# Performance work log

Measured on AMD Instinct MI355X. Metric: run time of the kernel, lower is better.

## Reference

```python
import jax, jax.numpy as jnp
import numpy as np

NUM_HEADS = 16
PROJECT_DIM = 1024
HEAD_DIM = PROJECT_DIM // NUM_HEADS  # 64; used only for the softmax scale


def setup_inputs() -> dict:
    key = jax.random.key(0)
    k1, k2, k3 = jax.random.split(key, 3)
    B, N, D = 8, 3072, PROJECT_DIM
    inputs = jax.random.normal(k1, (B, N, D), dtype=jnp.float32)
    wqkv = jax.random.normal(k2, (D, 3 * D), dtype=jnp.float32) * (1.0 / np.sqrt(D))
    dense_w = jax.random.normal(k3, (3 * D, D), dtype=jnp.float32) * (1.0 / np.sqrt(3 * D))
    dense_b = jnp.zeros((D,), dtype=jnp.float32)
    return {"inputs": inputs, "wqkv": wqkv, "dense_w": dense_w, "dense_b": dense_b}


def reference(inputs, wqkv, dense_w, dense_b):
    B, N, D = inputs.shape
    H = NUM_HEADS
    # fused QKV projection: [B, N, 3D]
    qkv = jnp.einsum('bnd,de->bne', inputs, wqkv)
    # separate heads: [B, H, N, 3*head_dim]
    qkv = qkv.reshape(B, N, H, (3 * D) // H).transpose(0, 2, 1, 3)
    # NOTE: faithful to source — split along TOKEN axis (axis=2) into 3 chunks
    q, k, v = jnp.split(qkv, 3, axis=2)  # each [B, H, N//3, 3*head_dim]
    scale = 1.0 / jnp.sqrt(jnp.float32(HEAD_DIM))
    logits = jnp.einsum('bhqc,bhkc->bhqk', q, k) * scale  # [B, H, N//3, N//3]
    attn = jax.nn.softmax(logits, axis=-1)
    out = jnp.einsum('bhqk,bhkc->bhqc', attn, v)  # [B, H, N//3, 3*head_dim]
    # recombine heads -> [B, N//3, 3D]
    out = out.transpose(0, 2, 1, 3).reshape(B, N // 3, 3 * D)
    # output projection -> [B, N//3, D]
    return jnp.einsum('bnc,cd->bnd', out, dense_w) + dense_b
```

## Files before the change

kernel.cpp:

```cpp
#include <hip/hip_runtime.h>
#include <hip/hip_bf16.h>

typedef unsigned short u16;
using f32x4  = __attribute__((ext_vector_type(4))) float;
using bf16x8 = __attribute__((ext_vector_type(8))) short;

typedef __attribute__((address_space(1))) const void global_cvoid;
typedef __attribute__((address_space(3))) void lds_void;

__device__ __forceinline__ void async16(const u16* g, u16* l) {
    __builtin_amdgcn_global_load_lds((global_cvoid*)g, (lds_void*)l, 16, 0, 0);
}

__device__ __forceinline__ u16 f2bf(float f) {
    union { float f; unsigned u; } cv; cv.f = f;
    unsigned r = cv.u + 0x7fff + ((cv.u >> 16) & 1);
    return (u16)(r >> 16);
}

__device__ __forceinline__ u16 f2bf_rz(float f) {
    union { float f; unsigned u; } cv; cv.f = f;
    return (u16)(cv.u >> 16);
}

__device__ __forceinline__ float dppmax16(float x) {
    union { float f; int i; } c, o;
    c.f = x;
    o.i = __builtin_amdgcn_update_dpp(0, c.i, 0xB1,  0xF, 0xF, true); c.f = fmaxf(c.f, o.f);
    o.i = __builtin_amdgcn_update_dpp(0, c.i, 0x4E,  0xF, 0xF, true); c.f = fmaxf(c.f, o.f);
    o.i = __builtin_amdgcn_update_dpp(0, c.i, 0x141, 0xF, 0xF, true); c.f = fmaxf(c.f, o.f);
    o.i = __builtin_amdgcn_update_dpp(0, c.i, 0x140, 0xF, 0xF, true); c.f = fmaxf(c.f, o.f);
    return c.f;
}
__device__ __forceinline__ float dppsum16(float x) {
    union { float f; int i; } c, o;
    c.f = x;
    o.i = __builtin_amdgcn_update_dpp(0, c.i, 0xB1,  0xF, 0xF, true); c.f += o.f;
    o.i = __builtin_amdgcn_update_dpp(0, c.i, 0x4E,  0xF, 0xF, true); c.f += o.f;
    o.i = __builtin_amdgcn_update_dpp(0, c.i, 0x141, 0xF, 0xF, true); c.f += o.f;
    o.i = __builtin_amdgcn_update_dpp(0, c.i, 0x140, 0xF, 0xF, true); c.f += o.f;
    return c.f;
}

__global__ __launch_bounds__(256) void cast_kernel(const float* __restrict__ src,
                                                   u16* __restrict__ dst, int n4) {
    int i = blockIdx.x * blockDim.x + threadIdx.x;
    int st = gridDim.x * blockDim.x;
    for (; i < n4; i += st) {
        float4 v = ((const float4*)src)[i];
        ushort4 o;
        o.x = f2bf(v.x); o.y = f2bf(v.y); o.z = f2bf(v.z); o.w = f2bf(v.w);
        ((ushort4*)dst)[i] = o;
    }
}

__global__ __launch_bounds__(256) void wtrans_kernel(const float* __restrict__ src,
                                                     u16* __restrict__ dst, int R, int C) {
    __shared__ float tile[64][68];
    int ct = blockIdx.x, rt = blockIdx.y;
    int t = threadIdx.x;
    int r = t >> 2;
    const float* s = src + (size_t)(rt * 64 + r) * C + ct * 64;
#pragma unroll
    for (int jj = 0; jj < 4; ++jj) {
        int c4 = (t & 3) + jj * 4;
        float4 v = *(const float4*)(s + c4 * 4);
        *(float4*)&tile[r][c4 * 4] = v;
    }
    __syncthreads();
    int od = t >> 2;
    u16* d = dst + (size_t)(ct * 64 + od) * R + rt * 64;
#pragma unroll
    for (int jj = 0; jj < 4; ++jj) {
        int c4 = (t & 3) + jj * 4;
        ushort4 v;
        v.x = f2bf(tile[c4 * 4 + 0][od]);
        v.y = f2bf(tile[c4 * 4 + 1][od]);
        v.z = f2bf(tile[c4 * 4 + 2][od]);
        v.w = f2bf(tile[c4 * 4 + 3][od]);
        *(ushort4*)(d + c4 * 4) = v;
    }
}

template<bool OUT_F32>
__global__ __launch_bounds__(256, 2)
void gemm_bt_kernel(const u16* __restrict__ A, const u16* __restrict__ BT,
                    void* __restrict__ Cout, const float* __restrict__ bias,
                    u16* __restrict__ VTout,
                    int M, int N, int K) {
    __shared__ u16 lA[128 * 64];
    __shared__ u16 lB[128 * 64];
    const int t = threadIdx.x;
    const int w = t >> 6, lane = t & 63;
    const int nbx = N >> 7;
    const int nwg = gridDim.x;
    int bid = blockIdx.x;
    int cpx = nwg >> 3;
    int swz = (bid & 7) * cpx + (bid >> 3);
    const int bx = swz % nbx;
    const int by = swz / nbx;
    const size_t m0 = (size_t)by * 128, n0 = (size_t)bx * 128;

    const int lr = lane >> 3;
    const int lc = (lane & 7) * 8;
    const int wr = (w >> 1) * 64, wc = (w & 1) * 64;

    f32x4 acc[4][4] = {};

    for (int kk = 0; kk < K; kk += 64) {
        __syncthreads();
#pragma unroll
        for (int i = 0; i < 4; ++i) {
            int rr = (w * 4 + i) * 8 + lr;
            async16(A  + (m0 + rr) * (size_t)K + kk + lc, &lA[(w * 4 + i) * 512]);
            async16(BT + (n0 + rr) * (size_t)K + kk + lc, &lB[(w * 4 + i) * 512]);
        }
        __syncthreads();
#pragma unroll
        for (int ks = 0; ks < 2; ++ks) {
            bf16x8 af[4], bfv[4];
#pragma unroll
            for (int m = 0; m < 4; ++m)
                af[m] = *(const bf16x8*)&lA[(wr + m * 16 + (lane & 15)) * 64 + ks * 32 + (lane >> 4) * 8];
#pragma unroll
            for (int n = 0; n < 4; ++n)
                bfv[n] = *(const bf16x8*)&lB[(wc + n * 16 + (lane & 15)) * 64 + ks * 32 + (lane >> 4) * 8];
#pragma unroll
            for (int m = 0; m < 4; ++m)
#pragma unroll
                for (int n = 0; n < 4; ++n)
                    acc[m][n] = __builtin_amdgcn_mfma_f32_16x16x32_bf16(af[m], bfv[n], acc[m][n], 0, 0, 0);
        }
    }

    const int r0 = (lane >> 4) * 4;
    const int cl = lane & 15;
    if constexpr (OUT_F32) {
        float* C = (float*)Cout;
#pragma unroll
        for (int m = 0; m < 4; ++m) {
            size_t row = m0 + wr + m * 16 + r0;
#pragma unroll
            for (int n = 0; n < 4; ++n) {
                size_t col = n0 + wc + n * 16 + cl;
                float bv = bias[col];
#pragma unroll
                for (int r = 0; r < 4; ++r)
                    C[(row + r) * (size_t)N + col] = acc[m][n][r] + bv;
            }
        }
    } else {
        int tok0 = (int)(m0 % 3072);
        if (VTout != nullptr && tok0 >= 2048) {
            int b = (int)(m0 / 3072);
#pragma unroll
            for (int m = 0; m < 4; ++m) {
                int tok = tok0 - 2048 + wr + m * 16 + r0;
#pragma unroll
                for (int n = 0; n < 4; ++n) {
                    int col = (int)n0 + wc + n * 16 + cl;
                    int h = col / 192, ch = col % 192;
                    ushort4 v;
                    v.x = f2bf(acc[m][n][0]);
                    v.y = f2bf(acc[m][n][1]);
                    v.z = f2bf(acc[m][n][2]);
                    v.w = f2bf(acc[m][n][3]);
                    *(ushort4*)(VTout + ((size_t)(b * 16 + h) * 192 + ch) * 1024 + tok) = v;
                }
            }
        } else {
            float qs = (VTout != nullptr && tok0 < 1024) ? 0.1803368801111f : 1.0f;
            u16* C = (u16*)Cout;
#pragma unroll
            for (int m = 0; m < 4; ++m) {
                size_t row = m0 + wr + m * 16 + r0;
#pragma unroll
                for (int n = 0; n < 4; ++n) {
                    size_t col = n0 + wc + n * 16 + cl;
#pragma unroll
                    for (int r = 0; r < 4; ++r)
                        C[(row + r) * (size_t)N + col] = f2bf(acc[m][n][r] * qs);
                }
            }
        }
    }
}

__global__ __launch_bounds__(256, 2)
void attn_kernel(const u16* __restrict__ QKV, const u16* __restrict__ VT,
                 u16* __restrict__ comb) {
    __shared__ u16 lds[32768];
    u16* lK = lds;
    u16* lV = lds + 12288;
    u16* lP = lds + 24576;

    const int t = threadIdx.x, w = t >> 6, lane = t & 63;
    const int bid = blockIdx.x;
    const int gid = (bid & 7) * 128 + (bid >> 3);
    const int bh = gid >> 3, qt = gid & 7;
    const int b = bh >> 4, h = bh & 15;

    const u16* Qg  = QKV + ((size_t)(b * 3072 + qt * 128 + w * 32)) * 3072 + h * 192;
    const u16* Kg  = QKV + ((size_t)(b * 3072 + 1024)) * 3072 + h * 192;
    const u16* VTg = VT + (size_t)bh * 192 * 1024;

    unsigned koff[6], voff[6];
#pragma unroll
    for (int i = 0; i < 6; ++i) {
        int ch = i * 256 + t;
        int kr = ch / 24, kc = ch % 24;
        koff[i] = kr * 3072 + (kc ^ (kr & 7)) * 8;
        int vr = ch >> 3, vc = ch & 7;
        voff[i] = vr * 1024 + (vc ^ (vr & 7)) * 8;
    }

#define STAGE_K(kt) do {                                                          \
    _Pragma("unroll")                                                             \
    for (int i = 0; i < 6; ++i)                                                   \
        async16(Kg + koff[i] + (unsigned)(kt) * 196608u, lK + (i * 256 + w * 64) * 8); \
    } while (0)
#define STAGE_V(kt) do {                                                          \
    _Pragma("unroll")                                                             \
    for (int i = 0; i < 6; ++i)                                                   \
        async16(VTg + voff[i] + (unsigned)(kt) * 64u, lV + (i * 256 + w * 64) * 8); \
    } while (0)

    STAGE_K(0);

    bf16x8 aq[2][6];
#pragma unroll
    for (int rg = 0; rg < 2; ++rg)
#pragma unroll
        for (int cs = 0; cs < 6; ++cs)
            aq[rg][cs] = *(const bf16x8*)(Qg + (size_t)(rg * 16 + (lane & 15)) * 3072
                                             + cs * 32 + (lane >> 4) * 8);

    f32x4 acc_o[2][12] = {};
    float m2[2][4], lsum[2][4];
#pragma unroll
    for (int rg = 0; rg < 2; ++rg)
#pragma unroll
        for (int r = 0; r < 4; ++r) { m2[rg][r] = -1e30f; lsum[rg][r] = 0.f; }
    u16* lPw = &lP[w * 2048];

#pragma unroll 1
    for (int it = 0; it < 16; ++it) {
        __syncthreads();
        STAGE_V(it);

        f32x4 s[2][4] = {};
        __builtin_amdgcn_s_setprio(1);
#pragma unroll
        for (int kf = 0; kf < 4; ++kf) {
            const int krow = kf * 16 + (lane & 15);
#pragma unroll
            for (int cs = 0; cs < 6; ++cs) {
                bf16x8 bk = *(const bf16x8*)&lK[krow * 192 + ((cs * 4 + (lane >> 4)) ^ (krow & 7)) * 8];
                s[0][kf] = __builtin_amdgcn_mfma_f32_16x16x32_bf16(aq[0][cs], bk, s[0][kf], 0, 0, 0);
                s[1][kf] = __builtin_amdgcn_mfma_f32_16x16x32_bf16(aq[1][cs], bk, s[1][kf], 0, 0, 0);
            }
        }
        __builtin_amdgcn_s_setprio(0);

#pragma unroll
        for (int rg = 0; rg < 2; ++rg) {
            float mx[4];
            bool need = false;
#pragma unroll
            for (int r = 0; r < 4; ++r) {
                float m = fmaxf(fmaxf(s[rg][0][r], s[rg][1][r]), fmaxf(s[rg][2][r], s[rg][3][r]));
                mx[r] = dppmax16(m);
                need = need || (mx[r] > m2[rg][r] + 8.f);
            }
            if (__any((int)need)) {
#pragma unroll
                for (int r = 0; r < 4; ++r) {
                    float mn = fmaxf(m2[rg][r], mx[r]);
                    float fac = exp2f(m2[rg][r] - mn);
                    m2[rg][r] = mn;
                    lsum[rg][r] *= fac;
#pragma unroll
                    for (int df = 0; df < 12; ++df) acc_o[rg][df][r] *= fac;
                }
            }
#pragma unroll
            for (int r = 0; r < 4; ++r) {
                int q = rg * 16 + (lane >> 4) * 4 + r;
                int xr = (q & 7) << 3;
                float rs = 0.f;
#pragma unroll
                for (int kf = 0; kf < 4; ++kf) {
                    float p = exp2f(s[rg][kf][r] - m2[rg][r]);
                    rs += p;
                    lPw[q * 64 + ((kf * 16 + (lane & 15)) ^ xr)] = f2bf_rz(p);
                }
                lsum[rg][r] += dppsum16(rs);
            }
        }

        __syncthreads();
        if (it + 1 < 16) STAGE_K(it + 1);

        __builtin_amdgcn_s_setprio(1);
#pragma unroll
        for (int ks = 0; ks < 2; ++ks) {
            const int prow0 = (lane & 15), prow1 = 16 + (lane & 15);
            const int pcol = ks * 32 + (lane >> 4) * 8;
            bf16x8 pa0 = *(const bf16x8*)&lPw[prow0 * 64 + (pcol ^ ((prow0 & 7) << 3))];
            bf16x8 pa1 = *(const bf16x8*)&lPw[(prow1) * 64 + (pcol ^ ((prow1 & 7) << 3))];
#pragma unroll
            for (int df = 0; df < 12; ++df) {
                const int vrow = df * 16 + (lane & 15);
                bf16x8 bv = *(const bf16x8*)&lV[vrow * 64 + ((ks * 4 + (lane >> 4)) ^ (vrow & 7)) * 8];
                acc_o[0][df] = __builtin_amdgcn_mfma_f32_16x16x32_bf16(pa0, bv, acc_o[0][df], 0, 0, 0);
                acc_o[1][df] = __builtin_amdgcn_mfma_f32_16x16x32_bf16(pa1, bv, acc_o[1][df], 0, 0, 0);
            }
        }
        __builtin_amdgcn_s_setprio(0);
    }

    u16* dst = comb + ((size_t)(b * 1024 + qt * 128 + w * 32)) * 3072 + h * 192;
#pragma unroll
    for (int rg = 0; rg < 2; ++rg)
#pragma unroll
        for (int r = 0; r < 4; ++r) {
            int q = rg * 16 + (lane >> 4) * 4 + r;
            float invl = 1.0f / lsum[rg][r];
#pragma unroll
            for (int df = 0; df < 12; ++df)
                dst[(size_t)q * 3072 + df * 16 + (lane & 15)] = f2bf(acc_o[rg][df][r] * invl);
        }
#undef STAGE_K
#undef STAGE_V
}

extern "C" void kernel_launch(void* const* d_in, const int* in_sizes, int n_in,
                              void* d_out, int out_size, void* d_ws, size_t ws_size,
                              hipStream_t stream) {
    const float* X  = (const float*)d_in[0];
    const float* W1 = (const float*)d_in[1];
    const float* W2 = (const float*)d_in[2];
    const float* Bb = (const float*)d_in[3];

    char* ws = (char*)d_ws;
    u16* Xb   = (u16*)(ws);
    u16* W1bT = (u16*)(ws + 50331648);
    u16* W2bT = (u16*)(ws + 56623104);
    u16* QKVb = (u16*)(ws + 62914560);
    u16* VT   = (u16*)(ws + 213909504);
    u16* comb = Xb;

    cast_kernel<<<2048, 256, 0, stream>>>(X, Xb, (8 * 3072 * 1024) / 4);
    wtrans_kernel<<<dim3(3072 / 64, 1024 / 64), 256, 0, stream>>>(W1, W1bT, 1024, 3072);
    wtrans_kernel<<<dim3(1024 / 64, 3072 / 64), 256, 0, stream>>>(W2, W2bT, 3072, 1024);
    gemm_bt_kernel<false><<<(24576 / 128) * (3072 / 128), 256, 0, stream>>>(
        Xb, W1bT, QKVb, nullptr, VT, 24576, 3072, 1024);
    attn_kernel<<<1024, 256, 0, stream>>>(QKVb, VT, comb);
    gemm_bt_kernel<true><<<(8192 / 128) * (1024 / 128), 256, 0, stream>>>(
        comb, W2bT, d_out, Bb, nullptr, 8192, 1024, 3072);
}
```

Before: 464.3 us.

## Add 256x256-tile 512-thread QKV GEMM kernel with 4-stage async LDS pipeline

Replaces the 128x128 QKV projection GEMM with a new 256x256-tile kernel using 8 waves, a 4-slot async global-to-LDS ring with swizzled layout, explicit vmcnt waits and s_setprio around the MFMA block. The larger tile doubles operand reuse per LDS load and cuts global traffic. The V-transpose and Q-scale epilogue moves into the new kernel, and the old kernel's epilogue is reduced to a plain bf16 store. Risks include higher register pressure (128 accumulator floats per lane), 128 KB of LDS per block, and fewer blocks for load balancing.

```diff
diff --git a/kernel.cpp b/kernel.cpp
--- a/kernel.cpp
+++ b/kernel.cpp
@@ -150,40 +150,130 @@
             }
         }
     } else {
-        int tok0 = (int)(m0 % 3072);
-        if (VTout != nullptr && tok0 >= 2048) {
-            int b = (int)(m0 / 3072);
-#pragma unroll
-            for (int m = 0; m < 4; ++m) {
-                int tok = tok0 - 2048 + wr + m * 16 + r0;
-#pragma unroll
-                for (int n = 0; n < 4; ++n) {
-                    int col = (int)n0 + wc + n * 16 + cl;
-                    int h = col / 192, ch = col % 192;
-                    ushort4 v;
-                    v.x = f2bf(acc[m][n][0]);
-                    v.y = f2bf(acc[m][n][1]);
-                    v.z = f2bf(acc[m][n][2]);
-                    v.w = f2bf(acc[m][n][3]);
-                    *(ushort4*)(VTout + ((size_t)(b * 16 + h) * 192 + ch) * 1024 + tok) = v;
-                }
-            }
-        } else {
-            float qs = (VTout != nullptr && tok0 < 1024) ? 0.1803368801111f : 1.0f;
-            u16* C = (u16*)Cout;
-#pragma unroll
-            for (int m = 0; m < 4; ++m) {
-                size_t row = m0 + wr + m * 16 + r0;
-#pragma unroll
-                for (int n = 0; n < 4; ++n) {
-                    size_t col = n0 + wc + n * 16 + cl;
-#pragma unroll
-                    for (int r = 0; r < 4; ++r)
-                        C[(row + r) * (size_t)N + col] = f2bf(acc[m][n][r] * qs);
-                }
-            }
-        }
-    }
+        u16* C = (u16*)Cout;
+#pragma unroll
+        for (int m = 0; m < 4; ++m) {
+            size_t row = m0 + wr + m * 16 + r0;
+#pragma unroll
+            for (int n = 0; n < 4; ++n) {
+                size_t col = n0 + wc + n * 16 + cl;
+#pragma unroll
+                for (int r = 0; r < 4; ++r)
+                    C[(row + r) * (size_t)N + col] = f2bf(acc[m][n][r]);
+            }
+        }
+    }
+}
+
+__global__ __launch_bounds__(512, 2)
+void gemm256_kernel(const u16* __restrict__ A, const u16* __restrict__ BT,
+                    u16* __restrict__ Cout, u16* __restrict__ VTout,
+                    int M, int N, int K) {
+    __shared__ u16 lds[65536];
+    u16* lA = lds;
+    u16* lB = lds + 32768;
+
+    const int t = threadIdx.x, w = t >> 6, l = t & 63;
+    const int g = l >> 4, ql = l & 15;
+    const int wm = w >> 2, wn = w & 3;
+    const int nbx = N >> 8;
+    int bid = blockIdx.x;
+    int cpx = gridDim.x >> 3;
+    int swz = (bid & 7) * cpx + (bid >> 3);
+    const int bx = swz % nbx, by = swz / nbx;
+    const size_t m0 = (size_t)by * 256, n0 = (size_t)bx * 256;
+
+    const u16* Ag = A  + m0 * (size_t)K;
+    const u16* Bg = BT + n0 * (size_t)K;
+
+    unsigned soff[2];
+#pragma unroll
+    for (int i = 0; i < 2; ++i) {
+        int ch = i * 512 + t;
+        int r = ch >> 2, c = ch & 3;
+        soff[i] = (unsigned)(r * K + (c ^ ((r >> 1) & 3)) * 8);
+    }
+
+#define STAGE8(kh3) do {                                                           \
+    int sl_ = (kh3) & 3;                                                           \
+    _Pragma("unroll")                                                              \
+    for (int i = 0; i < 2; ++i) {                                                  \
+        async16(Ag + soff[i] + (unsigned)(kh3) * 32u, lA + sl_ * 8192 + (i * 512 + w * 64) * 8); \
+        async16(Bg + soff[i] + (unsigned)(kh3) * 32u, lB + sl_ * 8192 + (i * 512 + w * 64) * 8); \
+    } } while (0)
+
+    STAGE8(0); STAGE8(1); STAGE8(2);
+
+    f32x4 acc[8][4] = {};
+    const int cswz = (g ^ ((ql >> 1) & 3)) * 8;
+    const int arow = wm * 128 + ql;
+    const int brow = wn * 64 + ql;
+
+    auto phase = [&](int kh, int vm, bool st) {
+        if (vm == 8)      asm volatile("s_waitcnt vmcnt(8)" ::: "memory");
+        else if (vm == 4) asm volatile("s_waitcnt vmcnt(4)" ::: "memory");
+        else              asm volatile("s_waitcnt vmcnt(0)" ::: "memory");
+        __builtin_amdgcn_s_barrier();
+        const u16* sA = lA + (kh & 3) * 8192;
+        const u16* sB = lB + (kh & 3) * 8192;
+        bf16x8 fa[8], fb[4];
+#pragma unroll
+        for (int m = 0; m < 8; ++m)
+            fa[m] = *(const bf16x8*)&sA[(arow + m * 16) * 32 + cswz];
+#pragma unroll
+        for (int n = 0; n < 4; ++n)
+            fb[n] = *(const bf16x8*)&sB[(brow + n * 16) * 32 + cswz];
+        if (st) STAGE8(kh + 3);
+        __builtin_amdgcn_s_setprio(1);
+#pragma unroll
+        for (int m = 0; m < 8; ++m)
+#pragma unroll
+            for (int n = 0; n < 4; ++n)
+                acc[m][n] = __builtin_amdgcn_mfma_f32_16x16x32_bf16(fa[m], fb[n], acc[m][n], 0, 0, 0);
+        __builtin_amdgcn_s_setprio(0);
+    };
+
+    const int KH = K >> 5;
+#pragma unroll 1
+    for (int kh = 0; kh < KH - 3; ++kh) phase(kh, 8, true);
+    phase(KH - 3, 8, false);
+    phase(KH - 2, 4, false);
+    phase(KH - 1, 0, false);
+
+    const int r0 = g * 4;
+    int tok0 = (int)(m0 % 3072);
+    if (tok0 >= 2048) {
+        int b = (int)(m0 / 3072);
+#pragma unroll
+        for (int m = 0; m < 8; ++m) {
+            int tok = tok0 - 2048 + wm * 128 + m * 16 + r0;
+#pragma unroll
+            for (int n = 0; n < 4; ++n) {
+                int col = (int)n0 + wn * 64 + n * 16 + ql;
+                int h = col / 192, ch = col % 192;
+                ushort4 v;
+                v.x = f2bf(acc[m][n][0]);
+                v.y = f2bf(acc[m][n][1]);
+                v.z = f2bf(acc[m][n][2]);
+                v.w = f2bf(acc[m][n][3]);
+                *(ushort4*)(VTout + ((size_t)(b * 16 + h) * 192 + ch) * 1024 + tok) = v;
+            }
+        }
+    } else {
+        float qs = (tok0 < 1024) ? 0.1803368801111f : 1.0f;
+#pragma unroll
+        for (int m = 0; m < 8; ++m) {
+            size_t row = m0 + wm * 128 + m * 16 + r0;
+#pragma unroll
+            for (int n = 0; n < 4; ++n) {
+                size_t col = n0 + wn * 64 + n * 16 + ql;
+#pragma unroll
+                for (int r = 0; r < 4; ++r)
+                    Cout[(row + r) * (size_t)N + col] = f2bf(acc[m][n][r] * qs);
+            }
+        }
+    }
+#undef STAGE8
 }
 
 __global__ __launch_bounds__(256, 2)
@@ -353,8 +443,8 @@
     cast_kernel<<<2048, 256, 0, stream>>>(X, Xb, (8 * 3072 * 1024) / 4);
     wtrans_kernel<<<dim3(3072 / 64, 1024 / 64), 256, 0, stream>>>(W1, W1bT, 1024, 3072);
     wtrans_kernel<<<dim3(1024 / 64, 3072 / 64), 256, 0, stream>>>(W2, W2bT, 3072, 1024);
-    gemm_bt_kernel<false><<<(24576 / 128) * (3072 / 128), 256, 0, stream>>>(
-        Xb, W1bT, QKVb, nullptr, VT, 24576, 3072, 1024);
+    gemm256_kernel<<<(24576 / 256) * (3072 / 256), 512, 0, stream>>>(
+        Xb, W1bT, QKVb, VT, 24576, 3072, 1024);
     attn_kernel<<<1024, 256, 0, stream>>>(QKVb, VT, comb);
     gemm_bt_kernel<true><<<(8192 / 128) * (1024 / 128), 256, 0, stream>>>(
         comb, W2bT, d_out, Bb, nullptr, 8192, 1024, 3072);
```

New measurement: 447.8 us. -3.6%, faster.
